# Optimization experiments

Measured on AMD Instinct MI355X. Metric: run time of the kernel, lower is better.

Reference implementation:

```python
import jax, jax.numpy as jnp
import numpy as np

C0 = 0.5 * np.sqrt(1.0 / np.pi)
C1 = np.sqrt(3.0 / (4 * np.pi))
C2 = 0.5 * np.sqrt(15.0 / (4 * np.pi))
C20 = 0.5 * np.sqrt(5.0 / (16 * np.pi))
C22 = 0.5 * np.sqrt(15.0 / (16 * np.pi))


def sh_basis(d):
    # d: [N,3] unit directions -> [N,9] (degree 2, matches torch code order)
    x, y, z = d[:, 0], d[:, 1], d[:, 2]
    return jnp.stack([
        C0 * jnp.ones_like(x),
        C1 * y, C1 * z, C1 * x,
        C2 * x * y, C2 * y * z,
        C20 * (3 * z * z - 1),
        C2 * x * z,
        C22 * (x * x - y * y),
    ], axis=-1)


def trilinear_sample(voxels, pts_norm):
    # voxels: [R,R,R,F] indexed (z,y,x); pts_norm: [N,3] in [-1,1] (x,y,z)
    # Matches F.grid_sample(align_corners=True, padding_mode='border').
    R = voxels.shape[0]
    c = jnp.clip((pts_norm + 1.0) * 0.5 * (R - 1), 0.0, R - 1)  # border clamp
    c0 = jnp.floor(c)
    f = c - c0                          # [N,3] fractional weights (fx,fy,fz)
    i0 = c0.astype(jnp.int32)
    i1 = jnp.minimum(i0 + 1, R - 1)
    x0, y0, z0 = i0[:, 0], i0[:, 1], i0[:, 2]
    x1, y1, z1 = i1[:, 0], i1[:, 1], i1[:, 2]
    fx, fy, fz = f[:, 0:1], f[:, 1:2], f[:, 2:3]
    g = lambda zi, yi, xi: voxels[zi, yi, xi]  # gather -> [N,F]
    c00 = g(z0, y0, x0) * (1 - fx) + g(z0, y0, x1) * fx
    c01 = g(z0, y1, x0) * (1 - fx) + g(z0, y1, x1) * fx
    c10 = g(z1, y0, x0) * (1 - fx) + g(z1, y0, x1) * fx
    c11 = g(z1, y1, x0) * (1 - fx) + g(z1, y1, x1) * fx
    c0_ = c00 * (1 - fy) + c01 * fy
    c1_ = c10 * (1 - fy) + c11 * fy
    return c0_ * (1 - fz) + c1_ * fz


def setup_inputs() -> dict:
    key = jax.random.key(0)
    k1, k2 = jax.random.split(key)
    N, R, F = 2_000_000, 192, 28
    points = jax.random.normal(k1, (N, 3), dtype=jnp.float32)
    voxels = jax.random.normal(k2, (R, R, R, F), dtype=jnp.float32) * 0.1
    return {"points": points, "voxels": voxels}


def reference(points, voxels):
    N = points.shape[0]
    sh_dim = 9
    pts_norm = points / 4.0
    feats = trilinear_sample(voxels, pts_norm)         # [N, 28]
    density = feats[:, 0]
    sh = feats[:, 1:].reshape(N, 3, sh_dim)            # [N,3,9]
    d = points / jnp.linalg.norm(points, axis=-1, keepdims=True)
    basis = sh_basis(d)[:, None, :]                    # [N,1,9]
    rgb = jax.nn.sigmoid(jnp.sum(sh * basis, axis=-1))  # [N,3]
    sigma = jax.nn.softplus(density)[:, None]           # [N,1]
    return rgb, sigma
```

## Files before the change

### kernel.cpp

```cpp
#include <hip/hip_runtime.h>
#include <math.h>

#define RDIM 192
#define FDIM 28
#define PPB 64

#define SH_C0  0.28209479177387814f
#define SH_C1  0.4886025119029199f
#define SH_C2  0.5462742152960396f
#define SH_C20 0.15769578262626154f
#define SH_C22 0.2731371076480198f

__global__ __launch_bounds__(256)
void plenoxel_fwd(const float* __restrict__ points,
                  const float* __restrict__ voxels,
                  float* __restrict__ out_rgb,
                  float* __restrict__ out_sigma,
                  int N)
{
    __shared__ float feats[PPB][FDIM];
    __shared__ float4 plds[PPB];

    const int tid   = threadIdx.x;
    const int group = tid >> 3;
    const int f     = tid & 7;
    const int pbase = blockIdx.x * PPB;
    const float4* __restrict__ src = (const float4*)voxels;

    const float A   = (RDIM - 1) / 8.0f;
    const float B   = (RDIM - 1) * 0.5f;
    const float RM1 = (float)(RDIM - 1);

    if (f < 7) {
#define POINT_SETUP(h, PIDX)                                                  \
        const int p##h  = (PIDX);                                             \
        const int cp##h = min(p##h, N - 1);                                   \
        const float px##h = points[3 * cp##h + 0];                            \
        const float py##h = points[3 * cp##h + 1];                            \
        const float pz##h = points[3 * cp##h + 2];                            \
        if (f == 0) plds[group + 32 * h] =                                    \
            make_float4(px##h, py##h, pz##h, 0.0f);                           \
        float cx##h = fminf(fmaxf(px##h * A + B, 0.0f), RM1);                 \
        float cy##h = fminf(fmaxf(py##h * A + B, 0.0f), RM1);                 \
        float cz##h = fminf(fmaxf(pz##h * A + B, 0.0f), RM1);                 \
        float fcx##h = floorf(cx##h), fcy##h = floorf(cy##h),                 \
              fcz##h = floorf(cz##h);                                         \
        float fx##h = cx##h - fcx##h, fy##h = cy##h - fcy##h,                 \
              fz##h = cz##h - fcz##h;                                         \
        int x0##h = (int)fcx##h, y0##h = (int)fcy##h, z0##h = (int)fcz##h;    \
        int x1##h = min(x0##h + 1, RDIM - 1);                                 \
        int y1##h = min(y0##h + 1, RDIM - 1);                                 \
        int z1##h = min(z0##h + 1, RDIM - 1);                                 \
        float gx##h = 1.0f - fx##h, gy##h = 1.0f - fy##h,                     \
              gz##h = 1.0f - fz##h;                                           \
        float w##h##0 = gz##h * gy##h * gx##h;                                \
        float w##h##1 = gz##h * gy##h * fx##h;                                \
        float w##h##2 = gz##h * fy##h * gx##h;                                \
        float w##h##3 = gz##h * fy##h * fx##h;                                \
        float w##h##4 = fz##h * gy##h * gx##h;                                \
        float w##h##5 = fz##h * gy##h * fx##h;                                \
        float w##h##6 = fz##h * fy##h * gx##h;                                \
        float w##h##7 = fz##h * fy##h * fx##h;                                \
        int a##h##0 = ((((z0##h * RDIM + y0##h) * RDIM + x0##h) * FDIM) >> 2) + f; \
        int a##h##1 = ((((z0##h * RDIM + y0##h) * RDIM + x1##h) * FDIM) >> 2) + f; \
        int a##h##2 = ((((z0##h * RDIM + y1##h) * RDIM + x0##h) * FDIM) >> 2) + f; \
        int a##h##3 = ((((z0##h * RDIM + y1##h) * RDIM + x1##h) * FDIM) >> 2) + f; \
        int a##h##4 = ((((z1##h * RDIM + y0##h) * RDIM + x0##h) * FDIM) >> 2) + f; \
        int a##h##5 = ((((z1##h * RDIM + y0##h) * RDIM + x1##h) * FDIM) >> 2) + f; \
        int a##h##6 = ((((z1##h * RDIM + y1##h) * RDIM + x0##h) * FDIM) >> 2) + f; \
        int a##h##7 = ((((z1##h * RDIM + y1##h) * RDIM + x1##h) * FDIM) >> 2) + f;

        POINT_SETUP(0, pbase + group)
        POINT_SETUP(1, pbase + group + 32)
#undef POINT_SETUP

        float4 v00 = src[a00]; float4 v01 = src[a01];
        float4 v02 = src[a02]; float4 v03 = src[a03];
        float4 v04 = src[a04]; float4 v05 = src[a05];
        float4 v06 = src[a06]; float4 v07 = src[a07];
        float4 v10 = src[a10]; float4 v11 = src[a11];
        float4 v12 = src[a12]; float4 v13 = src[a13];
        float4 v14 = src[a14]; float4 v15 = src[a15];
        float4 v16 = src[a16]; float4 v17 = src[a17];

#define ACC_STORE(h, V0, V1, V2, V3, V4, V5, V6, V7, ROW)                     \
        {                                                                     \
            float4 acc;                                                       \
            acc.x = w##h##0 * V0.x + w##h##1 * V1.x + w##h##2 * V2.x          \
                  + w##h##3 * V3.x + w##h##4 * V4.x + w##h##5 * V5.x          \
                  + w##h##6 * V6.x + w##h##7 * V7.x;                          \
            acc.y = w##h##0 * V0.y + w##h##1 * V1.y + w##h##2 * V2.y          \
                  + w##h##3 * V3.y + w##h##4 * V4.y + w##h##5 * V5.y          \
                  + w##h##6 * V6.y + w##h##7 * V7.y;                          \
            acc.z = w##h##0 * V0.z + w##h##1 * V1.z + w##h##2 * V2.z          \
                  + w##h##3 * V3.z + w##h##4 * V4.z + w##h##5 * V5.z          \
                  + w##h##6 * V6.z + w##h##7 * V7.z;                          \
            acc.w = w##h##0 * V0.w + w##h##1 * V1.w + w##h##2 * V2.w          \
                  + w##h##3 * V3.w + w##h##4 * V4.w + w##h##5 * V5.w          \
                  + w##h##6 * V6.w + w##h##7 * V7.w;                          \
            *(float4*)&feats[ROW][4 * f] = acc;                               \
        }

        ACC_STORE(0, v00, v01, v02, v03, v04, v05, v06, v07, group)
        ACC_STORE(1, v10, v11, v12, v13, v14, v15, v16, v17, group + 32)
#undef ACC_STORE
    }

    __syncthreads();

    if (tid < PPB) {
        int p2 = pbase + tid;
        if (p2 < N) {
            float4 pt = plds[tid];
            float px = pt.x, py = pt.y, pz = pt.z;

            float inv = rsqrtf(px * px + py * py + pz * pz);
            float dx = px * inv, dy = py * inv, dz = pz * inv;

            float basis[9];
            basis[0] = SH_C0;
            basis[1] = SH_C1 * dy;
            basis[2] = SH_C1 * dz;
            basis[3] = SH_C1 * dx;
            basis[4] = SH_C2 * dx * dy;
            basis[5] = SH_C2 * dy * dz;
            basis[6] = SH_C20 * (3.0f * dz * dz - 1.0f);
            basis[7] = SH_C2 * dx * dz;
            basis[8] = SH_C22 * (dx * dx - dy * dy);

#pragma unroll
            for (int c = 0; c < 3; ++c) {
                float s = 0.0f;
#pragma unroll
                for (int j = 0; j < 9; ++j) {
                    s += feats[tid][1 + 9 * c + j] * basis[j];
                }
                float r = 1.0f / (1.0f + expf(-s));
                __builtin_nontemporal_store(r, &out_rgb[3 * p2 + c]);
            }

            float x = feats[tid][0];
            float sig = fmaxf(x, 0.0f) + log1pf(expf(-fabsf(x)));
            __builtin_nontemporal_store(sig, &out_sigma[p2]);
        }
    }
}

extern "C" void kernel_launch(void* const* d_in, const int* in_sizes, int n_in,
                              void* d_out, int out_size, void* d_ws, size_t ws_size,
                              hipStream_t stream) {
    const float* points = (const float*)d_in[0];
    const float* voxels = (const float*)d_in[1];
    int N = in_sizes[0] / 3;

    float* out_rgb = (float*)d_out;
    float* out_sigma = out_rgb + (size_t)3 * N;

    int blocks = (N + PPB - 1) / PPB;
    plenoxel_fwd<<<blocks, 256, 0, stream>>>(points, voxels, out_rgb, out_sigma, N);
}
```

Baseline: 350.5 us.

## Gather x-adjacent voxel pairs as contiguous 16-lane loads and shuffle-reduce

Each point is now handled by 16 lanes instead of 8. Lanes 0-6 load the x0 voxel's 28 features and lanes 7-13 load the adjacent x1 voxel, which is contiguous in memory. This makes each (z,y) corner one contiguous 56-float read, cutting per-thread gathers from 8 to 4. Partial x-weighted sums are combined with a width-16 shuffle. It also drops the f<7 idle-lane branch, uses 4 points per thread, and adds shuffle and select overhead, with lanes 14-15 idle.

```diff
diff --git a/kernel.cpp b/kernel.cpp
--- a/kernel.cpp
+++ b/kernel.cpp
@@ -3,7 +3,8 @@
 
 #define RDIM 192
 #define FDIM 28
-#define PPB 64
+#define HPTS 4
+#define PPB  64
 
 #define SH_C0  0.28209479177387814f
 #define SH_C1  0.4886025119029199f
@@ -21,9 +22,9 @@
     __shared__ float feats[PPB][FDIM];
     __shared__ float4 plds[PPB];
 
-    const int tid   = threadIdx.x;
-    const int group = tid >> 3;
-    const int f     = tid & 7;
+    const int tid = threadIdx.x;
+    const int G   = tid >> 4;
+    const int l   = tid & 15;
     const int pbase = blockIdx.x * PPB;
     const float4* __restrict__ src = (const float4*)voxels;
 
@@ -31,80 +32,80 @@
     const float B   = (RDIM - 1) * 0.5f;
     const float RM1 = (float)(RDIM - 1);
 
-    if (f < 7) {
-#define POINT_SETUP(h, PIDX)                                                  \
-        const int p##h  = (PIDX);                                             \
-        const int cp##h = min(p##h, N - 1);                                   \
-        const float px##h = points[3 * cp##h + 0];                            \
-        const float py##h = points[3 * cp##h + 1];                            \
-        const float pz##h = points[3 * cp##h + 2];                            \
-        if (f == 0) plds[group + 32 * h] =                                    \
-            make_float4(px##h, py##h, pz##h, 0.0f);                           \
-        float cx##h = fminf(fmaxf(px##h * A + B, 0.0f), RM1);                 \
-        float cy##h = fminf(fmaxf(py##h * A + B, 0.0f), RM1);                 \
-        float cz##h = fminf(fmaxf(pz##h * A + B, 0.0f), RM1);                 \
-        float fcx##h = floorf(cx##h), fcy##h = floorf(cy##h),                 \
-              fcz##h = floorf(cz##h);                                         \
-        float fx##h = cx##h - fcx##h, fy##h = cy##h - fcy##h,                 \
-              fz##h = cz##h - fcz##h;                                         \
-        int x0##h = (int)fcx##h, y0##h = (int)fcy##h, z0##h = (int)fcz##h;    \
-        int x1##h = min(x0##h + 1, RDIM - 1);                                 \
-        int y1##h = min(y0##h + 1, RDIM - 1);                                 \
-        int z1##h = min(z0##h + 1, RDIM - 1);                                 \
-        float gx##h = 1.0f - fx##h, gy##h = 1.0f - fy##h,                     \
-              gz##h = 1.0f - fz##h;                                           \
-        float w##h##0 = gz##h * gy##h * gx##h;                                \
-        float w##h##1 = gz##h * gy##h * fx##h;                                \
-        float w##h##2 = gz##h * fy##h * gx##h;                                \
-        float w##h##3 = gz##h * fy##h * fx##h;                                \
-        float w##h##4 = fz##h * gy##h * gx##h;                                \
-        float w##h##5 = fz##h * gy##h * fx##h;                                \
-        float w##h##6 = fz##h * fy##h * gx##h;                                \
-        float w##h##7 = fz##h * fy##h * fx##h;                                \
-        int a##h##0 = ((((z0##h * RDIM + y0##h) * RDIM + x0##h) * FDIM) >> 2) + f; \
-        int a##h##1 = ((((z0##h * RDIM + y0##h) * RDIM + x1##h) * FDIM) >> 2) + f; \
-        int a##h##2 = ((((z0##h * RDIM + y1##h) * RDIM + x0##h) * FDIM) >> 2) + f; \
-        int a##h##3 = ((((z0##h * RDIM + y1##h) * RDIM + x1##h) * FDIM) >> 2) + f; \
-        int a##h##4 = ((((z1##h * RDIM + y0##h) * RDIM + x0##h) * FDIM) >> 2) + f; \
-        int a##h##5 = ((((z1##h * RDIM + y0##h) * RDIM + x1##h) * FDIM) >> 2) + f; \
-        int a##h##6 = ((((z1##h * RDIM + y1##h) * RDIM + x0##h) * FDIM) >> 2) + f; \
-        int a##h##7 = ((((z1##h * RDIM + y1##h) * RDIM + x1##h) * FDIM) >> 2) + f;
+#define POINT_SETUP(h)                                                        \
+    const int p##h  = pbase + G + 16 * h;                                     \
+    const int cp##h = min(p##h, N - 1);                                       \
+    const float px##h = points[3 * cp##h + 0];                                \
+    const float py##h = points[3 * cp##h + 1];                                \
+    const float pz##h = points[3 * cp##h + 2];                                \
+    if (l == 0) plds[G + 16 * h] = make_float4(px##h, py##h, pz##h, 0.0f);    \
+    float cx##h = fminf(fmaxf(px##h * A + B, 0.0f), RM1);                     \
+    float cy##h = fminf(fmaxf(py##h * A + B, 0.0f), RM1);                     \
+    float cz##h = fminf(fmaxf(pz##h * A + B, 0.0f), RM1);                     \
+    float fcx##h = floorf(cx##h), fcy##h = floorf(cy##h), fcz##h = floorf(cz##h); \
+    float fx##h = cx##h - fcx##h, fy##h = cy##h - fcy##h, fz##h = cz##h - fcz##h; \
+    int x0##h = (int)fcx##h, y0##h = (int)fcy##h, z0##h = (int)fcz##h;        \
+    int x1##h = min(x0##h + 1, RDIM - 1);                                     \
+    int y1##h = min(y0##h + 1, RDIM - 1);                                     \
+    int z1##h = min(z0##h + 1, RDIM - 1);                                     \
+    float gx##h = 1.0f - fx##h, gy##h = 1.0f - fy##h, gz##h = 1.0f - fz##h;   \
+    float wzy##h##0 = gz##h * gy##h;                                          \
+    float wzy##h##1 = gz##h * fy##h;                                          \
+    float wzy##h##2 = fz##h * gy##h;                                          \
+    float wzy##h##3 = fz##h * fy##h;                                          \
+                      \
+    int xo##h; {                                                              \
+        if (l < 7)       xo##h = l;                                           \
+        else if (l < 14) xo##h = (x1##h > x0##h) ? l : l - 7;                 \
+        else             xo##h = 0;                                           \
+    }                                                                         \
+    int a##h##0 = ((z0##h * RDIM + y0##h) * RDIM + x0##h) * 7 + xo##h;        \
+    int a##h##1 = ((z0##h * RDIM + y1##h) * RDIM + x0##h) * 7 + xo##h;        \
+    int a##h##2 = ((z1##h * RDIM + y0##h) * RDIM + x0##h) * 7 + xo##h;        \
+    int a##h##3 = ((z1##h * RDIM + y1##h) * RDIM + x0##h) * 7 + xo##h;
 
-        POINT_SETUP(0, pbase + group)
-        POINT_SETUP(1, pbase + group + 32)
+    POINT_SETUP(0)
+    POINT_SETUP(1)
+    POINT_SETUP(2)
+    POINT_SETUP(3)
 #undef POINT_SETUP
 
-        float4 v00 = src[a00]; float4 v01 = src[a01];
-        float4 v02 = src[a02]; float4 v03 = src[a03];
-        float4 v04 = src[a04]; float4 v05 = src[a05];
-        float4 v06 = src[a06]; float4 v07 = src[a07];
-        float4 v10 = src[a10]; float4 v11 = src[a11];
-        float4 v12 = src[a12]; float4 v13 = src[a13];
-        float4 v14 = src[a14]; float4 v15 = src[a15];
-        float4 v16 = src[a16]; float4 v17 = src[a17];
+    float4 v00 = src[a00]; float4 v01 = src[a01];
+    float4 v02 = src[a02]; float4 v03 = src[a03];
+    float4 v10 = src[a10]; float4 v11 = src[a11];
+    float4 v12 = src[a12]; float4 v13 = src[a13];
+    float4 v20 = src[a20]; float4 v21 = src[a21];
+    float4 v22 = src[a22]; float4 v23 = src[a23];
+    float4 v30 = src[a30]; float4 v31 = src[a31];
+    float4 v32 = src[a32]; float4 v33 = src[a33];
 
-#define ACC_STORE(h, V0, V1, V2, V3, V4, V5, V6, V7, ROW)                     \
-        {                                                                     \
-            float4 acc;                                                       \
-            acc.x = w##h##0 * V0.x + w##h##1 * V1.x + w##h##2 * V2.x          \
-                  + w##h##3 * V3.x + w##h##4 * V4.x + w##h##5 * V5.x          \
-                  + w##h##6 * V6.x + w##h##7 * V7.x;                          \
-            acc.y = w##h##0 * V0.y + w##h##1 * V1.y + w##h##2 * V2.y          \
-                  + w##h##3 * V3.y + w##h##4 * V4.y + w##h##5 * V5.y          \
-                  + w##h##6 * V6.y + w##h##7 * V7.y;                          \
-            acc.z = w##h##0 * V0.z + w##h##1 * V1.z + w##h##2 * V2.z          \
-                  + w##h##3 * V3.z + w##h##4 * V4.z + w##h##5 * V5.z          \
-                  + w##h##6 * V6.z + w##h##7 * V7.z;                          \
-            acc.w = w##h##0 * V0.w + w##h##1 * V1.w + w##h##2 * V2.w          \
-                  + w##h##3 * V3.w + w##h##4 * V4.w + w##h##5 * V5.w          \
-                  + w##h##6 * V6.w + w##h##7 * V7.w;                          \
-            *(float4*)&feats[ROW][4 * f] = acc;                               \
-        }
+#define REDUCE_STORE(h, V0, V1, V2, V3)                                       \
+    {                                                                         \
+        float wx = (l < 7) ? gx##h : fx##h;                                   \
+        float4 t;                                                             \
+        t.x = (wzy##h##0 * V0.x + wzy##h##1 * V1.x                            \
+             + wzy##h##2 * V2.x + wzy##h##3 * V3.x) * wx;                     \
+        t.y = (wzy##h##0 * V0.y + wzy##h##1 * V1.y                            \
+             + wzy##h##2 * V2.y + wzy##h##3 * V3.y) * wx;                     \
+        t.z = (wzy##h##0 * V0.z + wzy##h##1 * V1.z                            \
+             + wzy##h##2 * V2.z + wzy##h##3 * V3.z) * wx;                     \
+        t.w = (wzy##h##0 * V0.w + wzy##h##1 * V1.w                            \
+             + wzy##h##2 * V2.w + wzy##h##3 * V3.w) * wx;                     \
+        float sx = __shfl_down(t.x, 7, 16);                                   \
+        float sy = __shfl_down(t.y, 7, 16);                                   \
+        float sz = __shfl_down(t.z, 7, 16);                                   \
+        float sw = __shfl_down(t.w, 7, 16);                                   \
+        if (l < 7) {                                                          \
+            float4 r = make_float4(t.x + sx, t.y + sy, t.z + sz, t.w + sw);   \
+            *(float4*)&feats[G + 16 * h][4 * l] = r;                          \
+        }                                                                     \
+    }
 
-        ACC_STORE(0, v00, v01, v02, v03, v04, v05, v06, v07, group)
-        ACC_STORE(1, v10, v11, v12, v13, v14, v15, v16, v17, group + 32)
-#undef ACC_STORE
-    }
+    REDUCE_STORE(0, v00, v01, v02, v03)
+    REDUCE_STORE(1, v10, v11, v12, v13)
+    REDUCE_STORE(2, v20, v21, v22, v23)
+    REDUCE_STORE(3, v30, v31, v32, v33)
+#undef REDUCE_STORE
 
     __syncthreads();
 
```

Result: slower. 362.0 us (+3.3%).
